# Optimization experiments

Hardware: AMD Instinct MI355X
Metric: run time of the kernel (lower is better)

The kernel has to match this reference:

```python
import jax, jax.numpy as jnp
import numpy as np

B, T, F, U, M = 4096, 16, 512, 512, 8
OUT = 3
DELTA_T = 0.04

# ln_tau_table: tau starts at 1.0, multiplied by sqrt(10) each trace
_LN_TAU = np.log(1.0) + np.arange(M) * (0.5 * np.log(10.0))
LN_TAU = jnp.asarray(_LN_TAU, dtype=jnp.float32)          # (M,)
DECAY = jnp.exp(-DELTA_T / (jnp.exp(LN_TAU) + 1e-7))       # (M,)


def setup_inputs() -> dict:
    key = jax.random.key(0)
    ks = jax.random.split(key, 5)
    sc = 0.02
    return {
        "x": jax.random.normal(ks[0], (B, T, F), jnp.float32),
        "Wr": jax.random.normal(ks[1], (F + U, U * M), jnp.float32) * sc,
        "br": jnp.zeros((U * M,), jnp.float32),
        "Wq": jax.random.normal(ks[2], (F + U, U), jnp.float32) * sc,
        "bq": jnp.zeros((U,), jnp.float32),
        "Ws": jax.random.normal(ks[3], (F + U, U * M), jnp.float32) * sc,
        "bs": jnp.zeros((U * M,), jnp.float32),
        "Wo": jax.random.normal(ks[4], (U, OUT), jnp.float32) * sc,
        "bo": jnp.zeros((OUT,), jnp.float32),
    }


def _ctgru_forward(x, Wr, br, Wq, bq, Ws, bs, Wo, bo):
    def step(h_hat, xt):
        # h_hat: (B, U, M); xt: (B, F)
        h = h_hat.sum(axis=2)                              # (B, U)
        fused = jnp.concatenate([xt, h], axis=1)           # (B, F+U)
        ln_tau_r = (fused @ Wr + br).reshape(-1, U, M)
        r = jax.nn.softmax(-jnp.square(ln_tau_r - LN_TAU), axis=2)
        ctx = jnp.sum(r * h_hat, axis=2)                   # (B, U)
        q = jnp.tanh(jnp.concatenate([xt, ctx], axis=1) @ Wq + bq)[:, :, None]
        ln_tau_s = (fused @ Ws + bs).reshape(-1, U, M)
        s = jax.nn.softmax(-jnp.square(ln_tau_s - LN_TAU), axis=2)
        h_hat_next = ((1.0 - s) * h_hat + s * q) * DECAY   # (B, U, M)
        return h_hat_next, h_hat_next.sum(axis=2)          # carry, per-step hidden

    h0 = jnp.zeros((x.shape[0], U, M), x.dtype)
    _, hiddens = jax.lax.scan(step, h0, jnp.swapaxes(x, 0, 1))  # (T, B, U)
    hiddens = jnp.swapaxes(hiddens, 0, 1)                  # (B, T, U)
    return hiddens @ Wo + bo                               # (B, T, OUT)


def reference(x, Wr, br, Wq, bq, Ws, bs, Wo, bo):
    return _ctgru_forward(x, Wr, br, Wq, bq, Ws, bs, Wo, bo)
```

## Files before the change

kernel.cpp:

```cpp
#include <hip/hip_runtime.h>
#include <hip/hip_fp16.h>
#include <cmath>

#define Bdim 4096
#define Tdim 16
#define Fdim 512
#define Udim 512
#define Mdim 8
#define Kdim 1024

typedef __attribute__((ext_vector_type(8))) short bf16x8;
typedef __attribute__((ext_vector_type(4))) float f32x4;
typedef __attribute__((address_space(1))) const void* as1_cvp;
typedef __attribute__((address_space(3))) void* as3_vp;

__device__ __constant__ float c_lntau[8] = {
  0.0f, 1.15129254649702286f, 2.30258509299404572f, 3.45387763949106858f,
  4.60517018598809144f, 5.75646273248511430f, 6.90775527898213716f, 8.05904782547916002f
};
__device__ __constant__ float c_decay[8] = {
  0.96078944f, 0.98743055f, 0.99600799f, 0.99873589f,
  0.99960008f, 0.99987352f, 0.99996000f, 0.99998735f
};

__device__ __forceinline__ unsigned short f2bf(float f) {
  unsigned u = __float_as_uint(f);
  return (unsigned short)((u + 0x7fffu + ((u >> 16) & 1u)) >> 16);
}
__device__ __forceinline__ float bf2f(unsigned short h) {
  return __uint_as_float((unsigned)h << 16);
}
__device__ __forceinline__ void cvt_store8(float4 a, float4 b, short* ph, short* pl) {
  float f[8] = {a.x, a.y, a.z, a.w, b.x, b.y, b.z, b.w};
  bf16x8 hv, lv;
#pragma unroll
  for (int j = 0; j < 8; ++j) {
    unsigned short h = f2bf(f[j]);
    hv[j] = (short)h;
    lv[j] = (short)f2bf(f[j] - bf2f(h));
  }
  *(bf16x8*)ph = hv;
  *(bf16x8*)pl = lv;
}

#define GLOAD16(gp, lp) __builtin_amdgcn_global_load_lds((as1_cvp)(gp), (as3_vp)(lp), 16, 0, 0)

__global__ __launch_bounds__(256)
void wconv(const float* __restrict__ W, int ldw,
           short* __restrict__ WT_hi, short* __restrict__ WT_lo, int n_off)
{
  __shared__ float tile[64][65];
  const int tid = threadIdx.x;
  const int n0 = blockIdx.x * 64, k0 = blockIdx.y * 64;
#pragma unroll 4
  for (int i = 0; i < 16; ++i) {
    const int kl = i * 4 + (tid >> 6), nl = tid & 63;
    tile[kl][nl] = W[(size_t)(k0 + kl) * ldw + (n0 + nl)];
  }
  __syncthreads();
#pragma unroll 4
  for (int i = 0; i < 16; ++i) {
    const int nl = i * 4 + (tid >> 6), kl = tid & 63;
    const float v = tile[kl][nl];
    const unsigned short h = f2bf(v);
    const size_t di = (size_t)(n_off + n0 + nl) * 1024 + (k0 + kl);
    WT_hi[di] = (short)h;
    WT_lo[di] = (short)f2bf(v - bf2f(h));
  }
}

__device__ __forceinline__ void xsplit_row(const float* x, short* Ahw, short* Alw,
                                           int b, int t, int j)
{
  const float* s = x + ((size_t)b * Tdim + t) * Fdim + j * 8;
  const float4 a = *(const float4*)s;
  const float4 c = *(const float4*)(s + 4);
  cvt_store8(a, c, Ahw + (size_t)b * Kdim + j * 8, Alw + (size_t)b * Kdim + j * 8);
}

__global__ __launch_bounds__(64)
void xsplit0(const float* __restrict__ x, short* Ahw, short* Alw)
{
  xsplit_row(x, Ahw, Alw, blockIdx.x, 0, threadIdx.x);
}

__global__ __launch_bounds__(256)
void gemm_rs_mfma(const short* __restrict__ Ahg, const short* __restrict__ Alg,
                  const short* __restrict__ WTh, const short* __restrict__ WTl,
                  const float* __restrict__ br, const float* __restrict__ bs,
                  const float* __restrict__ h_hat, short* __restrict__ Ch,
                  short* __restrict__ Cl, __half* __restrict__ sbuf, int kmax)
{
  __shared__ short Ah[128 * 32], Al[128 * 32], Bh[128 * 32], Bl[128 * 32];
  const int tid = threadIdx.x, lane = tid & 63, wid = tid >> 6;
  const int m0 = blockIdx.y * 128, n0 = blockIdx.x * 128;
  const int wm = wid >> 1, wn = wid & 1;
  const int lrow16 = lane >> 2;
  const int lcb = (lane & 3) * 16;

  f32x4 acc[4][4];
#pragma unroll
  for (int i = 0; i < 4; ++i)
#pragma unroll
    for (int j = 0; j < 4; ++j) acc[i][j] = 0.0f;

  for (int k0 = 0; k0 < kmax; k0 += 32) {
    __syncthreads();
#pragma unroll
    for (int i = 0; i < 2; ++i) {
      const int rb = wid * 32 + i * 16;
      const size_t ga = ((size_t)(m0 + rb + lrow16) * Kdim + k0) * 2 + lcb;
      GLOAD16((const char*)Ahg + ga, (char*)Ah + rb * 64);
      GLOAD16((const char*)Alg + ga, (char*)Al + rb * 64);
      const size_t gw = ((size_t)(n0 + rb + lrow16) * Kdim + k0) * 2 + lcb;
      GLOAD16((const char*)WTh + gw, (char*)Bh + rb * 64);
      GLOAD16((const char*)WTl + gw, (char*)Bl + rb * 64);
    }
    __syncthreads();
    const int kg = lane >> 4, fr = lane & 15;
    bf16x8 ah[4], al[4], bh[4], bl[4];
#pragma unroll
    for (int mi = 0; mi < 4; ++mi) {
      const int row = wm * 64 + mi * 16 + fr;
      ah[mi] = *(const bf16x8*)&Ah[row * 32 + kg * 8];
      al[mi] = *(const bf16x8*)&Al[row * 32 + kg * 8];
    }
#pragma unroll
    for (int nj = 0; nj < 4; ++nj) {
      const int row = wn * 64 + nj * 16 + fr;
      bh[nj] = *(const bf16x8*)&Bh[row * 32 + kg * 8];
      bl[nj] = *(const bf16x8*)&Bl[row * 32 + kg * 8];
    }
#pragma unroll
    for (int mi = 0; mi < 4; ++mi)
#pragma unroll
      for (int nj = 0; nj < 4; ++nj) {
        acc[mi][nj] = __builtin_amdgcn_mfma_f32_16x16x32_bf16(ah[mi], bh[nj], acc[mi][nj], 0, 0, 0);
        acc[mi][nj] = __builtin_amdgcn_mfma_f32_16x16x32_bf16(ah[mi], bl[nj], acc[mi][nj], 0, 0, 0);
        acc[mi][nj] = __builtin_amdgcn_mfma_f32_16x16x32_bf16(al[mi], bh[nj], acc[mi][nj], 0, 0, 0);
      }
  }

  const bool is_s = (n0 >= Udim * Mdim);
  const float* bias = is_s ? bs : br;
  const int nb = is_s ? n0 - Udim * Mdim : n0;
  const float lnt = c_lntau[lane & 7];
  float bv[4];
#pragma unroll
  for (int nj = 0; nj < 4; ++nj) bv[nj] = bias[nb + wn * 64 + nj * 16 + (lane & 15)];

#pragma unroll
  for (int mi = 0; mi < 4; ++mi)
#pragma unroll
    for (int nj = 0; nj < 4; ++nj)
#pragma unroll
      for (int r = 0; r < 4; ++r) {
        const int brow = m0 + wm * 64 + mi * 16 + (lane >> 4) * 4 + r;
        const int ncol = nb + wn * 64 + nj * 16 + (lane & 15);
        const float v = acc[mi][nj][r] + bv[nj];
        const float d = v - lnt;
        float z = -d * d;
        float zm = z;
        zm = fmaxf(zm, __shfl_xor(zm, 1));
        zm = fmaxf(zm, __shfl_xor(zm, 2));
        zm = fmaxf(zm, __shfl_xor(zm, 4));
        const float e = expf(z - zm);
        float den = e;
        den += __shfl_xor(den, 1);
        den += __shfl_xor(den, 2);
        den += __shfl_xor(den, 4);
        const int u = ncol >> 3;
        if (!is_s) {
          const float hh = h_hat[((size_t)brow * Udim + u) * Mdim + (lane & 7)];
          float num = e * hh;
          num += __shfl_xor(num, 1);
          num += __shfl_xor(num, 2);
          num += __shfl_xor(num, 4);
          if ((lane & 7) == 0) {
            const float c = num / den;
            const unsigned short chh = f2bf(c);
            const size_t ci = (size_t)brow * Udim + u;
            Ch[ci] = (short)chh;
            Cl[ci] = (short)f2bf(c - bf2f(chh));
          }
        } else {
          sbuf[((size_t)brow * Udim + u) * Mdim + (lane & 7)] = __float2half(e / den);
        }
      }
}

__global__ __launch_bounds__(256)
void gemm_q_mfma(const short* Ahg, const short* Alg,
                 const short* Chg, const short* Clg,
                 const float* __restrict__ Wq, const float* __restrict__ bq,
                 const __half* __restrict__ sbuf, float* __restrict__ h_hat,
                 short* Ahw, short* Alw, int kmax)
{
  __shared__ short Ah[64 * 32], Al[64 * 32], Bh[128 * 32], Bl[128 * 32];
  const int tid = threadIdx.x, lane = tid & 63, wid = tid >> 6;
  const int m0 = blockIdx.y * 64, n0 = blockIdx.x * 128;
  const int wm = wid >> 1, wn = wid & 1;
  const int lrow16 = lane >> 2, lcb = (lane & 3) * 16;
  const int kr = tid & 31, ng = tid >> 5;

  f32x4 acc[2][4];
#pragma unroll
  for (int i = 0; i < 2; ++i)
#pragma unroll
    for (int j = 0; j < 4; ++j) acc[i][j] = 0.0f;

  for (int k0 = 0; k0 < kmax; k0 += 32) {
    __syncthreads();
    {
      const int rb = wid * 16;
      if (k0 < Fdim) {
        const size_t ga = ((size_t)(m0 + rb + lrow16) * Kdim + k0) * 2 + lcb;
        GLOAD16((const char*)Ahg + ga, (char*)Ah + rb * 64);
        GLOAD16((const char*)Alg + ga, (char*)Al + rb * 64);
      } else {
        const size_t ga = ((size_t)(m0 + rb + lrow16) * Udim + (k0 - Fdim)) * 2 + lcb;
        GLOAD16((const char*)Chg + ga, (char*)Ah + rb * 64);
        GLOAD16((const char*)Clg + ga, (char*)Al + rb * 64);
      }
    }
    {
      const float* wp = Wq + (size_t)(k0 + kr) * Udim + n0 + ng * 16;
      const float4 w0 = *(const float4*)wp,      w1 = *(const float4*)(wp + 4);
      const float4 w2 = *(const float4*)(wp + 8), w3 = *(const float4*)(wp + 12);
      const float wv[16] = {w0.x, w0.y, w0.z, w0.w, w1.x, w1.y, w1.z, w1.w,
                            w2.x, w2.y, w2.z, w2.w, w3.x, w3.y, w3.z, w3.w};
#pragma unroll
      for (int i2 = 0; i2 < 16; ++i2) {
        const unsigned short hh = f2bf(wv[i2]);
        Bh[(ng * 16 + i2) * 32 + kr] = (short)hh;
        Bl[(ng * 16 + i2) * 32 + kr] = (short)f2bf(wv[i2] - bf2f(hh));
      }
    }
    __syncthreads();
    const int kg = lane >> 4, fr = lane & 15;
    bf16x8 ah[2], al[2], bh[4], bl[4];
#pragma unroll
    for (int mi = 0; mi < 2; ++mi) {
      const int row = wm * 32 + mi * 16 + fr;
      ah[mi] = *(const bf16x8*)&Ah[row * 32 + kg * 8];
      al[mi] = *(const bf16x8*)&Al[row * 32 + kg * 8];
    }
#pragma unroll
    for (int nj = 0; nj < 4; ++nj) {
      const int row = wn * 64 + nj * 16 + fr;
      bh[nj] = *(const bf16x8*)&Bh[row * 32 + kg * 8];
      bl[nj] = *(const bf16x8*)&Bl[row * 32 + kg * 8];
    }
#pragma unroll
    for (int mi = 0; mi < 2; ++mi)
#pragma unroll
      for (int nj = 0; nj < 4; ++nj) {
        acc[mi][nj] = __builtin_amdgcn_mfma_f32_16x16x32_bf16(ah[mi], bh[nj], acc[mi][nj], 0, 0, 0);
        acc[mi][nj] = __builtin_amdgcn_mfma_f32_16x16x32_bf16(ah[mi], bl[nj], acc[mi][nj], 0, 0, 0);
        acc[mi][nj] = __builtin_amdgcn_mfma_f32_16x16x32_bf16(al[mi], bh[nj], acc[mi][nj], 0, 0, 0);
      }
  }

  float bv[4];
#pragma unroll
  for (int nj = 0; nj < 4; ++nj) bv[nj] = bq[n0 + wn * 64 + nj * 16 + (lane & 15)];

#pragma unroll
  for (int mi = 0; mi < 2; ++mi)
#pragma unroll
    for (int nj = 0; nj < 4; ++nj)
#pragma unroll
      for (int r = 0; r < 4; ++r) {
        const int b = m0 + wm * 32 + mi * 16 + (lane >> 4) * 4 + r;
        const int u = n0 + wn * 64 + nj * 16 + (lane & 15);
        const float qv = tanhf(acc[mi][nj][r] + bv[nj]);
        const size_t base = ((size_t)b * Udim + u) * Mdim;
        const __half2* sp = (const __half2*)(sbuf + base);
        const __half2 s01 = sp[0], s23 = sp[1], s45 = sp[2], s67 = sp[3];
        const float sv[8] = {__low2float(s01), __high2float(s01), __low2float(s23), __high2float(s23),
                             __low2float(s45), __high2float(s45), __low2float(s67), __high2float(s67)};
        const float4 h0 = *(const float4*)(h_hat + base);
        const float4 h1 = *(const float4*)(h_hat + base + 4);
        float hv[8] = {h0.x, h0.y, h0.z, h0.w, h1.x, h1.y, h1.z, h1.w};
        float sum = 0.f;
#pragma unroll
        for (int m = 0; m < 8; ++m) {
          const float nh = ((1.0f - sv[m]) * hv[m] + sv[m] * qv) * c_decay[m];
          hv[m] = nh;
          sum += nh;
        }
        *(float4*)(h_hat + base)     = make_float4(hv[0], hv[1], hv[2], hv[3]);
        *(float4*)(h_hat + base + 4) = make_float4(hv[4], hv[5], hv[6], hv[7]);
        const unsigned short sh = f2bf(sum);
        Ahw[(size_t)b * Kdim + Fdim + u] = (short)sh;
        Alw[(size_t)b * Kdim + Fdim + u] = (short)f2bf(sum - bf2f(sh));
      }
}

__global__ __launch_bounds__(64)
void out_step(const short* Ahg, const short* Alg,
              const float* __restrict__ Wo, const float* __restrict__ bo,
              float* __restrict__ out, const float* __restrict__ x,
              short* Ahw, short* Alw, int t)
{
  const int b = blockIdx.x, lane = threadIdx.x;
  const short* hh = Ahg + (size_t)b * Kdim + Fdim;
  const short* hl = Alg + (size_t)b * Kdim + Fdim;
  float a0 = 0.f, a1 = 0.f, a2 = 0.f;
#pragma unroll
  for (int u0 = 0; u0 < Udim; u0 += 64) {
    const int u = u0 + lane;
    const float hv = bf2f((unsigned short)hh[u]) + bf2f((unsigned short)hl[u]);
    const float* w = Wo + (size_t)u * 3;
    a0 = fmaf(hv, w[0], a0);
    a1 = fmaf(hv, w[1], a1);
    a2 = fmaf(hv, w[2], a2);
  }
#pragma unroll
  for (int off = 32; off; off >>= 1) {
    a0 += __shfl_down(a0, off);
    a1 += __shfl_down(a1, off);
    a2 += __shfl_down(a2, off);
  }
  if (lane == 0) {
    float* o = out + ((size_t)b * Tdim + t) * 3;
    o[0] = a0 + bo[0]; o[1] = a1 + bo[1]; o[2] = a2 + bo[2];
  }
  if (t + 1 < Tdim) xsplit_row(x, Ahw, Alw, b, t + 1, lane);
}

__global__ __launch_bounds__(256)
void zero_kernel(float4* __restrict__ p, size_t n4)
{
  const size_t i = (size_t)blockIdx.x * 256 + threadIdx.x;
  const size_t stride = (size_t)gridDim.x * 256;
  for (size_t j = i; j < n4; j += stride)
    p[j] = make_float4(0.f, 0.f, 0.f, 0.f);
}

extern "C" void kernel_launch(void* const* d_in, const int* in_sizes, int n_in,
                              void* d_out, int out_size, void* d_ws, size_t ws_size,
                              hipStream_t stream)
{
  const float* x  = (const float*)d_in[0];
  const float* Wr = (const float*)d_in[1];
  const float* br = (const float*)d_in[2];
  const float* Wq = (const float*)d_in[3];
  const float* bq = (const float*)d_in[4];
  const float* Ws = (const float*)d_in[5];
  const float* bs = (const float*)d_in[6];
  const float* Wo = (const float*)d_in[7];
  const float* bo = (const float*)d_in[8];
  float* out = (float*)d_out;

  const size_t need = 159383552;
  if (ws_size < need) return;

  char* p = (char*)d_ws;
  short* WTh = (short*)p;  p += 16777216;
  short* WTl = (short*)p;  p += 16777216;
  short* Ahg = (short*)p;  p += 8388608;
  short* Alg = (short*)p;  p += 8388608;
  short* Ch  = (short*)p;  p += 4194304;
  short* Cl  = (short*)p;  p += 4194304;
  float* hhat = (float*)p; p += 67108864;
  __half* sbuf = (__half*)p;

  zero_kernel<<<2048, 256, 0, stream>>>((float4*)hhat, 4194304);
  wconv<<<dim3(64, 16), 256, 0, stream>>>(Wr, 4096, WTh, WTl, 0);
  wconv<<<dim3(64, 16), 256, 0, stream>>>(Ws, 4096, WTh, WTl, 4096);
  xsplit0<<<4096, 64, 0, stream>>>(x, Ahg, Alg);

  for (int t = 0; t < Tdim; ++t) {
    const int kmax = t ? Kdim : Fdim;
    gemm_rs_mfma<<<dim3(64, 32), 256, 0, stream>>>(Ahg, Alg, WTh, WTl, br, bs,
                                                   hhat, Ch, Cl, sbuf, kmax);
    gemm_q_mfma<<<dim3(4, 64), 256, 0, stream>>>(Ahg, Alg, Ch, Cl, Wq, bq,
                                                 sbuf, hhat, Ahg, Alg, kmax);
    out_step<<<4096, 64, 0, stream>>>(Ahg, Alg, Wo, bo, out, x, Ahg, Alg, t);
  }
}
```

Baseline: 6.619 ms.

## Double-buffer LDS tiles in both MFMA GEMM kernels to overlap loads with compute

```diff
diff --git a/kernel.cpp b/kernel.cpp
--- a/kernel.cpp
+++ b/kernel.cpp
@@ -91,7 +91,8 @@
                   const float* __restrict__ h_hat, short* __restrict__ Ch,
                   short* __restrict__ Cl, __half* __restrict__ sbuf, int kmax)
 {
-  __shared__ short Ah[128 * 32], Al[128 * 32], Bh[128 * 32], Bl[128 * 32];
+  __shared__ short Ah[2 * 128 * 32], Al[2 * 128 * 32];
+  __shared__ short Bh[2 * 128 * 32], Bl[2 * 128 * 32];
   const int tid = threadIdx.x, lane = tid & 63, wid = tid >> 6;
   const int m0 = blockIdx.y * 128, n0 = blockIdx.x * 128;
   const int wm = wid >> 1, wn = wid & 1;
@@ -104,32 +105,40 @@
 #pragma unroll
     for (int j = 0; j < 4; ++j) acc[i][j] = 0.0f;
 
-  for (int k0 = 0; k0 < kmax; k0 += 32) {
-    __syncthreads();
+  auto STAGE = [&](int buf, int k0) {
+    const int boff = buf * (128 * 32);
 #pragma unroll
     for (int i = 0; i < 2; ++i) {
       const int rb = wid * 32 + i * 16;
       const size_t ga = ((size_t)(m0 + rb + lrow16) * Kdim + k0) * 2 + lcb;
-      GLOAD16((const char*)Ahg + ga, (char*)Ah + rb * 64);
-      GLOAD16((const char*)Alg + ga, (char*)Al + rb * 64);
+      GLOAD16((const char*)Ahg + ga, (char*)(Ah + boff) + rb * 64);
+      GLOAD16((const char*)Alg + ga, (char*)(Al + boff) + rb * 64);
       const size_t gw = ((size_t)(n0 + rb + lrow16) * Kdim + k0) * 2 + lcb;
-      GLOAD16((const char*)WTh + gw, (char*)Bh + rb * 64);
-      GLOAD16((const char*)WTl + gw, (char*)Bl + rb * 64);
-    }
-    __syncthreads();
+      GLOAD16((const char*)WTh + gw, (char*)(Bh + boff) + rb * 64);
+      GLOAD16((const char*)WTl + gw, (char*)(Bl + boff) + rb * 64);
+    }
+  };
+
+  STAGE(0, 0);
+  __syncthreads();
+  int cur = 0;
+
+  for (int k0 = 0; k0 < kmax; k0 += 32) {
+    if (k0 + 32 < kmax) STAGE(cur ^ 1, k0 + 32);
+    const int boff = cur * (128 * 32);
     const int kg = lane >> 4, fr = lane & 15;
     bf16x8 ah[4], al[4], bh[4], bl[4];
 #pragma unroll
     for (int mi = 0; mi < 4; ++mi) {
       const int row = wm * 64 + mi * 16 + fr;
-      ah[mi] = *(const bf16x8*)&Ah[row * 32 + kg * 8];
-      al[mi] = *(const bf16x8*)&Al[row * 32 + kg * 8];
+      ah[mi] = *(const bf16x8*)&Ah[boff + row * 32 + kg * 8];
+      al[mi] = *(const bf16x8*)&Al[boff + row * 32 + kg * 8];
     }
 #pragma unroll
     for (int nj = 0; nj < 4; ++nj) {
       const int row = wn * 64 + nj * 16 + fr;
-      bh[nj] = *(const bf16x8*)&Bh[row * 32 + kg * 8];
-      bl[nj] = *(const bf16x8*)&Bl[row * 32 + kg * 8];
+      bh[nj] = *(const bf16x8*)&Bh[boff + row * 32 + kg * 8];
+      bl[nj] = *(const bf16x8*)&Bl[boff + row * 32 + kg * 8];
     }
 #pragma unroll
     for (int mi = 0; mi < 4; ++mi)
@@ -139,6 +148,8 @@
         acc[mi][nj] = __builtin_amdgcn_mfma_f32_16x16x32_bf16(ah[mi], bl[nj], acc[mi][nj], 0, 0, 0);
         acc[mi][nj] = __builtin_amdgcn_mfma_f32_16x16x32_bf16(al[mi], bh[nj], acc[mi][nj], 0, 0, 0);
       }
+    __syncthreads();
+    cur ^= 1;
   }
 
   const bool is_s = (n0 >= Udim * Mdim);
@@ -196,7 +207,8 @@
                  const __half* __restrict__ sbuf, float* __restrict__ h_hat,
                  short* Ahw, short* Alw, int kmax)
 {
-  __shared__ short Ah[64 * 32], Al[64 * 32], Bh[128 * 32], Bl[128 * 32];
+  __shared__ short Ah[2 * 64 * 32], Al[2 * 64 * 32];
+  __shared__ short Bh[2 * 128 * 32], Bl[2 * 128 * 32];
   const int tid = threadIdx.x, lane = tid & 63, wid = tid >> 6;
   const int m0 = blockIdx.y * 64, n0 = blockIdx.x * 128;
   const int wm = wid >> 1, wn = wid & 1;
@@ -209,47 +221,56 @@
 #pragma unroll
     for (int j = 0; j < 4; ++j) acc[i][j] = 0.0f;
 
-  for (int k0 = 0; k0 < kmax; k0 += 32) {
-    __syncthreads();
+  auto STAGE = [&](int buf, int k0) {
     {
+      const int aoff = buf * (64 * 32);
       const int rb = wid * 16;
       if (k0 < Fdim) {
         const size_t ga = ((size_t)(m0 + rb + lrow16) * Kdim + k0) * 2 + lcb;
-        GLOAD16((const char*)Ahg + ga, (char*)Ah + rb * 64);
-        GLOAD16((const char*)Alg + ga, (char*)Al + rb * 64);
+        GLOAD16((const char*)Ahg + ga, (char*)(Ah + aoff) + rb * 64);
+        GLOAD16((const char*)Alg + ga, (char*)(Al + aoff) + rb * 64);
       } else {
         const size_t ga = ((size_t)(m0 + rb + lrow16) * Udim + (k0 - Fdim)) * 2 + lcb;
-        GLOAD16((const char*)Chg + ga, (char*)Ah + rb * 64);
-        GLOAD16((const char*)Clg + ga, (char*)Al + rb * 64);
+        GLOAD16((const char*)Chg + ga, (char*)(Ah + aoff) + rb * 64);
+        GLOAD16((const char*)Clg + ga, (char*)(Al + aoff) + rb * 64);
       }
     }
     {
+      const int boff = buf * (128 * 32);
       const float* wp = Wq + (size_t)(k0 + kr) * Udim + n0 + ng * 16;
-      const float4 w0 = *(const float4*)wp,      w1 = *(const float4*)(wp + 4);
+      const float4 w0 = *(const float4*)wp,       w1 = *(const float4*)(wp + 4);
       const float4 w2 = *(const float4*)(wp + 8), w3 = *(const float4*)(wp + 12);
       const float wv[16] = {w0.x, w0.y, w0.z, w0.w, w1.x, w1.y, w1.z, w1.w,
                             w2.x, w2.y, w2.z, w2.w, w3.x, w3.y, w3.z, w3.w};
 #pragma unroll
       for (int i2 = 0; i2 < 16; ++i2) {
         const unsigned short hh = f2bf(wv[i2]);
-        Bh[(ng * 16 + i2) * 32 + kr] = (short)hh;
-        Bl[(ng * 16 + i2) * 32 + kr] = (short)f2bf(wv[i2] - bf2f(hh));
-      }
-    }
-    __syncthreads();
+        Bh[boff + (ng * 16 + i2) * 32 + kr] = (short)hh;
+        Bl[boff + (ng * 16 + i2) * 32 + kr] = (short)f2bf(wv[i2] - bf2f(hh));
+      }
+    }
+  };
+
+  STAGE(0, 0);
+  __syncthreads();
+  int cur = 0;
+
+  for (int k0 = 0; k0 < kmax; k0 += 32) {
+    if (k0 + 32 < kmax) STAGE(cur ^ 1, k0 + 32);
+    const int aoff = cur * (64 * 32), boff = cur * (128 * 32);
     const int kg = lane >> 4, fr = lane & 15;
     bf16x8 ah[2], al[2], bh[4], bl[4];
 #pragma unroll
     for (int mi = 0; mi < 2; ++mi) {
       const int row = wm * 32 + mi * 16 + fr;
-      ah[mi] = *(const bf16x8*)&Ah[row * 32 + kg * 8];
-      al[mi] = *(const bf16x8*)&Al[row * 32 + kg * 8];
+      ah[mi] = *(const bf16x8*)&Ah[aoff + row * 32 + kg * 8];
+      al[mi] = *(const bf16x8*)&Al[aoff + row * 32 + kg * 8];
     }
 #pragma unroll
     for (int nj = 0; nj < 4; ++nj) {
       const int row = wn * 64 + nj * 16 + fr;
-      bh[nj] = *(const bf16x8*)&Bh[row * 32 + kg * 8];
-      bl[nj] = *(const bf16x8*)&Bl[row * 32 + kg * 8];
+      bh[nj] = *(const bf16x8*)&Bh[boff + row * 32 + kg * 8];
+      bl[nj] = *(const bf16x8*)&Bl[boff + row * 32 + kg * 8];
     }
 #pragma unroll
     for (int mi = 0; mi < 2; ++mi)
@@ -259,6 +280,8 @@
         acc[mi][nj] = __builtin_amdgcn_mfma_f32_16x16x32_bf16(ah[mi], bl[nj], acc[mi][nj], 0, 0, 0);
         acc[mi][nj] = __builtin_amdgcn_mfma_f32_16x16x32_bf16(al[mi], bh[nj], acc[mi][nj], 0, 0, 0);
       }
+    __syncthreads();
+    cur ^= 1;
   }
 
   float bv[4];
```

Result: no change. 6.691 ms (+1.1%).
